# Optimization experiments

Hardware: AMD Instinct MI355X
Metric: run time of the kernel (lower is better)

## Reference

```python
import jax, jax.numpy as jnp
import numpy as np

A, N, D, H, ADIM = 8, 32768, 128, 4, 32  # agents, batch, hidden, heads, attend_dim


def setup_inputs() -> dict:
    key = jax.random.key(0)
    ks = jax.random.split(key, 7)
    querys = jax.random.normal(ks[0], (A, N, D), jnp.float32)
    keys = jax.random.normal(ks[1], (A, N, D), jnp.float32)
    values = jax.random.normal(ks[2], (A, N, D), jnp.float32)
    s = 1.0 / np.sqrt(D)
    Wk = jax.random.normal(ks[3], (H, ADIM, D), jnp.float32) * s   # key_extractors (no bias)
    Wsel = jax.random.normal(ks[4], (H, ADIM, D), jnp.float32) * s  # selector_extractors (no bias)
    Wv = jax.random.normal(ks[5], (H, ADIM, D), jnp.float32) * s   # value_extractors Linear
    bv = jax.random.normal(ks[6], (H, ADIM), jnp.float32) * s      # value_extractors bias
    return {"querys": querys, "keys": keys, "values": values,
            "Wk": Wk, "Wsel": Wsel, "Wv": Wv, "bv": bv}


def _offdiag_idx(a):
    # idx[i, j] enumerates the a-1 agents != i, in order (matches torch list comp j != a_i)
    j = jnp.arange(a - 1)[None, :]
    i = jnp.arange(a)[:, None]
    return jnp.where(j < i, j, j + 1)  # [A, A-1]


def reference(querys, keys, values, Wk, Wsel, Wv, bv):
    # per-head projections: [H, A, N, K]
    hk = jnp.einsum('and,hkd->hank', keys, Wk)
    hs = jnp.einsum('and,hkd->hank', querys, Wsel)
    hv = jax.nn.leaky_relu(jnp.einsum('and,hkd->hank', values, Wv) + bv[:, None, None, :],
                           negative_slope=0.01)
    # full logits over all key-agents j for each query-agent i: [H, A, N, A]
    logits_full = jnp.einsum('hink,hjnk->hinj', hs, hk)
    scale = 1.0 / jnp.sqrt(jnp.asarray(hk.shape[-1], hk.dtype))
    # self-exclusion: mask j == i so softmax over j equals softmax over the other agents
    self_mask = jnp.eye(A, dtype=bool)[None, :, None, :]
    probs_full = jax.nn.softmax(jnp.where(self_mask, -1e9, logits_full * scale), axis=-1)
    # attended values: [H, A, N, K] (diagonal prob is exactly 0 after masking? it is ~e^{-1e9} ~ 0)
    other = jnp.einsum('hinj,hjnk->hink', probs_full, hv)
    # gather the self-excluded logits/probs in the original (A-1)-length layout
    idx = _offdiag_idx(A)
    idx4 = jnp.broadcast_to(idx[None, :, None, :], logits_full.shape[:-1] + (A - 1,))
    logits_ex = jnp.take_along_axis(logits_full, idx4, axis=-1)  # [H, A, N, A-1]
    probs_ex = jnp.take_along_axis(probs_full, idx4, axis=-1)    # [H, A, N, A-1]
    # reorder to agent-major like the torch nested lists: [A, H, ...]
    return (jnp.swapaxes(other, 0, 1),
            jnp.swapaxes(logits_ex, 0, 1),
            jnp.swapaxes(probs_ex, 0, 1))
```

## Files before the change

kernel.cpp:

```cpp
#include <hip/hip_runtime.h>
#include <hip/hip_bf16.h>

typedef unsigned short u16;
typedef unsigned int u32;

#define AGT 8
#define NBATCH 32768
#define DDIM 128
#define HEADS 4
#define KDIM 32

typedef float f32x4 __attribute__((ext_vector_type(4)));
typedef __bf16 bf16x8 __attribute__((ext_vector_type(8)));
typedef short s16x8 __attribute__((ext_vector_type(8)));
typedef u32 u32x4 __attribute__((ext_vector_type(4)));

union FragU { s16x8 s; bf16x8 b; u32x4 u; };

__device__ __forceinline__ u16 f2bf(float f) {
  u32 u = __float_as_uint(f);
  u = (u + 0x7FFFu + ((u >> 16) & 1u)) >> 16;
  return (u16)u;
}

__global__ void prep_weights(const float* __restrict__ Wk,
                             const float* __restrict__ Ws,
                             const float* __restrict__ Wv,
                             u16* __restrict__ Wb) {
  int idx = blockIdx.x * 256 + threadIdx.x;
  if (idx >= 3 * 8 * 4 * 64 * 8) return;
  int b  = idx & 7;
  int l  = (idx >> 3) & 63;
  int kc = (idx >> 9) & 3;
  int t  = (idx >> 11) & 7;
  int pj = idx >> 14;
  int c = t * 16 + (l & 15);
  int h = c >> 5, kk = c & 31;
  int d = kc * 32 + ((b >> 2) << 4) + ((l >> 4) << 2) + (b & 3);
  const float* W = (pj == 0) ? Wk : ((pj == 1) ? Ws : Wv);
  Wb[idx] = f2bf(W[(h * KDIM + kk) * DDIM + d]);
}

__device__ __forceinline__ void issue8(const float* __restrict__ rowp, int lg,
                                       float4 r[8]) {
#pragma unroll
  for (int kc = 0; kc < 4; ++kc) {
    r[kc * 2]     = *(const float4*)(rowp + kc * 32 + lg * 4);
    r[kc * 2 + 1] = *(const float4*)(rowp + kc * 32 + lg * 4 + 16);
  }
}

__device__ __forceinline__ void cvt8(const float4 r[8], FragU f[4]) {
#pragma unroll
  for (int kc = 0; kc < 4; ++kc) {
    const float4 x0 = r[kc * 2];
    const float4 x1 = r[kc * 2 + 1];
    FragU t;
    t.b[0] = (__bf16)x0.x; t.b[1] = (__bf16)x0.y;
    t.b[2] = (__bf16)x0.z; t.b[3] = (__bf16)x0.w;
    t.b[4] = (__bf16)x1.x; t.b[5] = (__bf16)x1.y;
    t.b[6] = (__bf16)x1.z; t.b[7] = (__bf16)x1.w;
    f[kc] = t;
  }
}

__device__ __forceinline__ FragU pack2(const f32x4 lo, const f32x4 hi) {
  FragU t;
  t.b[0] = (__bf16)lo[0]; t.b[1] = (__bf16)lo[1];
  t.b[2] = (__bf16)lo[2]; t.b[3] = (__bf16)lo[3];
  t.b[4] = (__bf16)hi[0]; t.b[5] = (__bf16)hi[1];
  t.b[6] = (__bf16)hi[2]; t.b[7] = (__bf16)hi[3];
  return t;
}

template <int PJ>
__device__ __forceinline__ void projT2(const FragU fx0[4], const FragU fx1[4],
                                       const u16* __restrict__ Wb, int l,
                                       FragU o0[HEADS], FragU o1[HEADS]) {
  const f32x4 z = (f32x4)(0.0f);
#pragma unroll
  for (int g = 0; g < 2; ++g) {
    f32x4 a0[4], a1[4];
#pragma unroll
    for (int m4 = 0; m4 < 4; ++m4) {
      a0[m4] = z;
      a1[m4] = z;
      const int mt = g * 4 + m4;
#pragma unroll
      for (int kc = 0; kc < 4; ++kc) {
        FragU fb;
        fb.s = *(const s16x8*)(Wb + ((((PJ * 8 + mt) * 4 + kc) * 64 + l) << 3));
        a0[m4] = __builtin_amdgcn_mfma_f32_16x16x32_bf16(fb.b, fx0[kc].b,
                                                         a0[m4], 0, 0, 0);
        a1[m4] = __builtin_amdgcn_mfma_f32_16x16x32_bf16(fb.b, fx1[kc].b,
                                                         a1[m4], 0, 0, 0);
      }
    }
#pragma unroll
    for (int hh = 0; hh < 2; ++hh) {
      o0[g * 2 + hh] = pack2(a0[2 * hh], a0[2 * hh + 1]);
      o1[g * 2 + hh] = pack2(a1[2 * hh], a1[2 * hh + 1]);
    }
  }
}

__device__ __forceinline__ void projV2(const FragU fx0[4], const FragU fx1[4],
                                       const u16* __restrict__ Wb, int l,
                                       const float biasr[8],
                                       u32 hv0[8][2], u32 hv1[8][2]) {
  const f32x4 z = (f32x4)(0.0f);
#pragma unroll
  for (int ct = 0; ct < 8; ++ct) {
    f32x4 a0 = z, a1 = z;
#pragma unroll
    for (int kc = 0; kc < 4; ++kc) {
      FragU fb;
      fb.s = *(const s16x8*)(Wb + ((((16 + ct) * 4 + kc) * 64 + l) << 3));
      a0 = __builtin_amdgcn_mfma_f32_16x16x32_bf16(fx0[kc].b, fb.b, a0, 0, 0, 0);
      a1 = __builtin_amdgcn_mfma_f32_16x16x32_bf16(fx1[kc].b, fb.b, a1, 0, 0, 0);
    }
    const float bb = biasr[ct];
    {
      float x0 = a0[0] + bb, x1 = a0[1] + bb, x2 = a0[2] + bb, x3 = a0[3] + bb;
      x0 = (x0 > 0.f) ? x0 : 0.01f * x0;
      x1 = (x1 > 0.f) ? x1 : 0.01f * x1;
      x2 = (x2 > 0.f) ? x2 : 0.01f * x2;
      x3 = (x3 > 0.f) ? x3 : 0.01f * x3;
      FragU t;
      t.b[0] = (__bf16)x0; t.b[1] = (__bf16)x1;
      t.b[2] = (__bf16)x2; t.b[3] = (__bf16)x3;
      hv0[ct][0] = t.u[0];
      hv0[ct][1] = t.u[1];
    }
    {
      float x0 = a1[0] + bb, x1 = a1[1] + bb, x2 = a1[2] + bb, x3 = a1[3] + bb;
      x0 = (x0 > 0.f) ? x0 : 0.01f * x0;
      x1 = (x1 > 0.f) ? x1 : 0.01f * x1;
      x2 = (x2 > 0.f) ? x2 : 0.01f * x2;
      x3 = (x3 > 0.f) ? x3 : 0.01f * x3;
      FragU t;
      t.b[0] = (__bf16)x0; t.b[1] = (__bf16)x1;
      t.b[2] = (__bf16)x2; t.b[3] = (__bf16)x3;
      hv1[ct][0] = t.u[0];
      hv1[ct][1] = t.u[1];
    }
  }
}

__global__ __launch_bounds__(256, 3) void fused_attn(
    const float* __restrict__ qin, const float* __restrict__ kin,
    const float* __restrict__ vin, const u16* __restrict__ Wb,
    const float* __restrict__ bv,
    float* __restrict__ out0, float* __restrict__ out1,
    float* __restrict__ out2) {
  const int tid = threadIdx.x;
  const int l = tid & 63;
  const int w = tid >> 6;
  const int lr = l & 15;
  const int lg = l >> 4;
  const int nbase = (blockIdx.x * 4 + w) * 4;
  const int my_agent = lr >> 1;
  const int ipar = lr & 1;
  const size_t xoff0 =
      ((size_t)my_agent * NBATCH + (size_t)(nbase + ipar)) * DDIM;
  const size_t xoff1 = xoff0 + 2 * DDIM;

  float biasr[8];
#pragma unroll
  for (int ct = 0; ct < 8; ++ct) biasr[ct] = bv[ct * 16 + lr];

  const f32x4 zero4 = (f32x4)(0.0f);
  const float scale = 0.17677669529663687f;

  FragU hk[2][HEADS], hs[2][HEADS];
  u32 hv[2][8][2];

  {
    float4 rA[8], rB[8];
    issue8(kin + xoff0, lg, rA);
    issue8(kin + xoff1, lg, rB);
    FragU fx0[4], fx1[4];
    cvt8(rA, fx0);
    cvt8(rB, fx1);
    projT2<0>(fx0, fx1, Wb, l, hk[0], hk[1]);
  }
  {
    float4 rA[8], rB[8];
    issue8(qin + xoff0, lg, rA);
    issue8(qin + xoff1, lg, rB);
    FragU fx0[4], fx1[4];
    cvt8(rA, fx0);
    cvt8(rB, fx1);
    projT2<1>(fx0, fx1, Wb, l, hs[0], hs[1]);
  }
  {
    float4 rA[8], rB[8];
    issue8(vin + xoff0, lg, rA);
    issue8(vin + xoff1, lg, rB);
    FragU fx0[4], fx1[4];
    cvt8(rA, fx0);
    cvt8(rB, fx1);
    projV2(fx0, fx1, Wb, l, biasr, hv[0], hv[1]);
  }

  f32x4 S[2][HEADS];
#pragma unroll
  for (int t = 0; t < 2; ++t)
#pragma unroll
    for (int h = 0; h < HEADS; ++h)
      S[t][h] = __builtin_amdgcn_mfma_f32_16x16x32_bf16(hk[t][h].b, hs[t][h].b,
                                                        zero4, 0, 0, 0);

  const int a_i = my_agent;
#pragma unroll
  for (int t = 0; t < 2; ++t) {
    const int n_i = nbase + 2 * t + ipar;
#pragma unroll
    for (int h = 0; h < HEADS; ++h) {
      float sl[4];
#pragma unroll
      for (int rg = 0; rg < 4; ++rg) {
        const int jrow = 4 * lg + rg;
        const bool valid = ((rg & 1) == ipar) && (jrow != lr);
        sl[rg] = valid ? S[t][h][rg] * scale : -1e30f;
      }
      float mp = fmaxf(fmaxf(sl[0], sl[1]), fmaxf(sl[2], sl[3]));
      mp = fmaxf(mp, __shfl_xor(mp, 16));
      mp = fmaxf(mp, __shfl_xor(mp, 32));
      float e[4];
      float sp = 0.0f;
#pragma unroll
      for (int rg = 0; rg < 4; ++rg) {
        e[rg] = __expf(sl[rg] - mp);
        sp += e[rg];
      }
      sp += __shfl_xor(sp, 16);
      sp += __shfl_xor(sp, 32);
      const float inv = 1.0f / sp;
      float p[4];
#pragma unroll
      for (int rg = 0; rg < 4; ++rg) p[rg] = e[rg] * inv;

      const size_t ob7 =
          ((size_t)(a_i * HEADS + h) * NBATCH + (size_t)n_i) * 7;
#pragma unroll
      for (int rg = 0; rg < 4; ++rg) {
        const int jrow = 4 * lg + rg;
        if (((rg & 1) == ipar) && (jrow != lr)) {
          const int a_j = jrow >> 1;
          const int jj = a_j - ((a_j > a_i) ? 1 : 0);
          out1[ob7 + jj] = S[t][h][rg];
          out2[ob7 + jj] = p[rg];
        }
      }

      FragU P;
      P.b[0] = (__bf16)p[0]; P.b[1] = (__bf16)p[1];
      P.b[2] = (__bf16)p[2]; P.b[3] = (__bf16)p[3];
      P.u[2] = 0;
      P.u[3] = 0;
      FragU B0, B1;
      B0.u[0] = hv[t][2 * h][0];     B0.u[1] = hv[t][2 * h][1];
      B0.u[2] = 0;                   B0.u[3] = 0;
      B1.u[0] = hv[t][2 * h + 1][0]; B1.u[1] = hv[t][2 * h + 1][1];
      B1.u[2] = 0;                   B1.u[3] = 0;
      f32x4 O0 = __builtin_amdgcn_mfma_f32_16x16x32_bf16(P.b, B0.b, zero4,
                                                         0, 0, 0);
      f32x4 O1 = __builtin_amdgcn_mfma_f32_16x16x32_bf16(P.b, B1.b, zero4,
                                                         0, 0, 0);
#pragma unroll
      for (int rg = 0; rg < 4; ++rg) {
        const int irow = 4 * lg + rg;
        const int a_o = irow >> 1;
        const int n_o = nbase + 2 * t + (irow & 1);
        const size_t o0 =
            ((size_t)(a_o * HEADS + h) * NBATCH + (size_t)n_o) * KDIM;
        out0[o0 + lr] = O0[rg];
        out0[o0 + 16 + lr] = O1[rg];
      }
    }
  }
}

extern "C" void kernel_launch(void* const* d_in, const int* in_sizes, int n_in,
                              void* d_out, int out_size, void* d_ws,
                              size_t ws_size, hipStream_t stream) {
  const float* qin = (const float*)d_in[0];
  const float* kin = (const float*)d_in[1];
  const float* vin = (const float*)d_in[2];
  const float* Wk  = (const float*)d_in[3];
  const float* Ws  = (const float*)d_in[4];
  const float* Wv  = (const float*)d_in[5];
  const float* bvp = (const float*)d_in[6];

  float* out0 = (float*)d_out;
  float* out1 = out0 + (size_t)AGT * HEADS * NBATCH * KDIM;
  float* out2 = out1 + (size_t)AGT * HEADS * NBATCH * 7;

  u16* Wb = (u16*)d_ws;

  prep_weights<<<dim3(192), dim3(256), 0, stream>>>(Wk, Ws, Wv, Wb);
  fused_attn<<<dim3(2048), dim3(256), 0, stream>>>(
      qin, kin, vin, Wb, bvp, out0, out1, out2);
}
```

Before: 232.2 us.

## Split fused attention into projection and attention kernels via bf16 workspace

```diff
diff --git a/kernel.cpp b/kernel.cpp
--- a/kernel.cpp
+++ b/kernel.cpp
@@ -11,6 +11,7 @@
 #define KDIM 32
 
 typedef float f32x4 __attribute__((ext_vector_type(4)));
+typedef float f32x2 __attribute__((ext_vector_type(2)));
 typedef __bf16 bf16x8 __attribute__((ext_vector_type(8)));
 typedef short s16x8 __attribute__((ext_vector_type(8)));
 typedef u32 u32x4 __attribute__((ext_vector_type(4)));
@@ -21,6 +22,13 @@
   u32 u = __float_as_uint(f);
   u = (u + 0x7FFFu + ((u >> 16) & 1u)) >> 16;
   return (u16)u;
+}
+
+__device__ __forceinline__ f32x2 bfpair(u32 u) {
+  f32x2 r;
+  r.x = __uint_as_float(u << 16);
+  r.y = __uint_as_float(u & 0xFFFF0000u);
+  return r;
 }
 
 __global__ void prep_weights(const float* __restrict__ Wk,
@@ -64,6 +72,156 @@
   }
 }
 
+__global__ __launch_bounds__(256, 4) void proj_kernel(
+    const float* __restrict__ qin, const float* __restrict__ kin,
+    const float* __restrict__ vin, const u16* __restrict__ Wb,
+    const float* __restrict__ bv, u16* __restrict__ Y) {
+  const int tid = threadIdx.x;
+  const int l = tid & 63;
+  const int w = tid >> 6;
+  const int lr = l & 15;
+  const int lg = l >> 4;
+
+  const int gw = blockIdx.x * 4 + w;
+  const int pj = gw >> 13;
+  const int tile = gw & 8191;
+  const int r0 = tile * 32;
+  const int a = r0 >> 15;
+  const int n0 = r0 & (NBATCH - 1);
+
+  const float* X = (pj == 0) ? kin : ((pj == 1) ? qin : vin);
+  u16* Yp = Y + (size_t)pj * ((size_t)NBATCH * AGT * 128);
+
+  float4 rA[8], rB[8];
+  issue8(X + (size_t)(r0 + lr) * DDIM, lg, rA);
+  issue8(X + (size_t)(r0 + 16 + lr) * DDIM, lg, rB);
+  FragU fx0[4], fx1[4];
+  cvt8(rA, fx0);
+  cvt8(rB, fx1);
+
+  const f32x4 z = (f32x4)(0.0f);
+  const float bias = (pj == 2) ? bv[0 * 16 + lr] : 0.0f;
+
+#pragma unroll
+  for (int ct = 0; ct < 8; ++ct) {
+    f32x4 a0 = z, a1 = z;
+#pragma unroll
+    for (int kc = 0; kc < 4; ++kc) {
+      FragU fb;
+      fb.s = *(const s16x8*)(Wb + ((((pj * 8 + ct) * 4 + kc) * 64 + l) << 3));
+      a0 = __builtin_amdgcn_mfma_f32_16x16x32_bf16(fx0[kc].b, fb.b, a0, 0, 0, 0);
+      a1 = __builtin_amdgcn_mfma_f32_16x16x32_bf16(fx1[kc].b, fb.b, a1, 0, 0, 0);
+    }
+    const int c = ct * 16 + lr;
+    if (pj == 2) {
+      const float bb = bv[c];
+#pragma unroll
+      for (int rg = 0; rg < 4; ++rg) {
+        float v0 = a0[rg] + bb;
+        a0[rg] = (v0 > 0.f) ? v0 : 0.01f * v0;
+        float v1 = a1[rg] + bb;
+        a1[rg] = (v1 > 0.f) ? v1 : 0.01f * v1;
+      }
+    }
+#pragma unroll
+    for (int rg = 0; rg < 4; ++rg) {
+      const int row = 4 * lg + rg;
+      Yp[((size_t)(n0 + row) * 8 + a) * 128 + c] = f2bf(a0[rg]);
+      Yp[((size_t)(n0 + 16 + row) * 8 + a) * 128 + c] = f2bf(a1[rg]);
+    }
+  }
+  (void)bias;
+}
+
+__global__ __launch_bounds__(256, 4) void attn_kernel(
+    const u16* __restrict__ Y, float* __restrict__ out0,
+    float* __restrict__ out1, float* __restrict__ out2) {
+  const int tid = threadIdx.x;
+  const int i = tid & 7;
+  const int h = (tid >> 3) & 3;
+  const int n = blockIdx.x * 8 + (tid >> 5);
+
+  const size_t PST = (size_t)NBATCH * AGT * 128;
+  const u16* Yk = Y;
+  const u16* Ys = Y + PST;
+  const u16* Yv = Y + 2 * PST;
+  const int cb = h * 32;
+
+  f32x2 hs2[16];
+  {
+    const u16* p = Ys + ((size_t)n * 8 + i) * 128 + cb;
+#pragma unroll
+    for (int q = 0; q < 4; ++q) {
+      u32x4 ch = *(const u32x4*)(p + q * 8);
+#pragma unroll
+      for (int e = 0; e < 4; ++e) hs2[q * 4 + e] = bfpair(ch[e]);
+    }
+  }
+
+  float logits[8];
+#pragma unroll
+  for (int j = 0; j < 8; ++j) {
+    const u16* p = Yk + ((size_t)n * 8 + j) * 128 + cb;
+    f32x2 a2 = (f32x2)(0.0f);
+#pragma unroll
+    for (int q = 0; q < 4; ++q) {
+      u32x4 ch = *(const u32x4*)(p + q * 8);
+#pragma unroll
+      for (int e = 0; e < 4; ++e) a2 = bfpair(ch[e]) * hs2[q * 4 + e] + a2;
+    }
+    logits[j] = a2.x + a2.y;
+  }
+
+  const float scale = 0.17677669529663687f;
+  float sl[8];
+#pragma unroll
+  for (int j = 0; j < 8; ++j) sl[j] = (j == i) ? -1e30f : logits[j] * scale;
+  float m = sl[0];
+#pragma unroll
+  for (int j = 1; j < 8; ++j) m = fmaxf(m, sl[j]);
+  float p[8];
+  float s = 0.0f;
+#pragma unroll
+  for (int j = 0; j < 8; ++j) { p[j] = __expf(sl[j] - m); s += p[j]; }
+  const float inv = 1.0f / s;
+
+  const size_t ob = ((size_t)(i * HEADS + h) * NBATCH + (size_t)n);
+  const size_t ob7 = ob * 7;
+#pragma unroll
+  for (int j = 0; j < 8; ++j) {
+    if (j != i) {
+      const int jj = j - ((j > i) ? 1 : 0);
+      out1[ob7 + jj] = logits[j];
+      out2[ob7 + jj] = p[j] * inv;
+    }
+  }
+
+  f32x2 o2[16];
+#pragma unroll
+  for (int e = 0; e < 16; ++e) o2[e] = (f32x2)(0.0f);
+#pragma unroll
+  for (int j = 0; j < 8; ++j) {
+    const float pw = p[j] * inv;
+    const f32x2 pw2 = (f32x2)(pw);
+    const u16* vp = Yv + ((size_t)n * 8 + j) * 128 + cb;
+#pragma unroll
+    for (int q = 0; q < 4; ++q) {
+      u32x4 ch = *(const u32x4*)(vp + q * 8);
+#pragma unroll
+      for (int e = 0; e < 4; ++e)
+        o2[q * 4 + e] = bfpair(ch[e]) * pw2 + o2[q * 4 + e];
+    }
+  }
+
+  const size_t o0 = ob * 32;
+#pragma unroll
+  for (int g = 0; g < 8; ++g) {
+    float4 vv = make_float4(o2[g * 2].x, o2[g * 2].y,
+                            o2[g * 2 + 1].x, o2[g * 2 + 1].y);
+    *(float4*)(out0 + o0 + g * 4) = vv;
+  }
+}
+
 __device__ __forceinline__ FragU pack2(const f32x4 lo, const f32x4 hi) {
   FragU t;
   t.b[0] = (__bf16)lo[0]; t.b[1] = (__bf16)lo[1];
@@ -147,7 +305,7 @@
   }
 }
 
-__global__ __launch_bounds__(256, 3) void fused_attn(
+__global__ __launch_bounds__(256, 3) void fused_attn_fb(
     const float* __restrict__ qin, const float* __restrict__ kin,
     const float* __restrict__ vin, const u16* __restrict__ Wb,
     const float* __restrict__ bv,
@@ -298,8 +456,20 @@
   float* out2 = out1 + (size_t)AGT * HEADS * NBATCH * 7;
 
   u16* Wb = (u16*)d_ws;
+  const size_t WB_ELEMS = 49152;
+  const size_t Y_ELEMS = (size_t)3 * NBATCH * AGT * 128;
+  const size_t NEED = (WB_ELEMS + Y_ELEMS) * sizeof(u16);
 
   prep_weights<<<dim3(192), dim3(256), 0, stream>>>(Wk, Ws, Wv, Wb);
-  fused_attn<<<dim3(2048), dim3(256), 0, stream>>>(
-      qin, kin, vin, Wb, bvp, out0, out1, out2);
-}
+
+  if (ws_size >= NEED) {
+    u16* Y = Wb + WB_ELEMS;
+    proj_kernel<<<dim3(6144), dim3(256), 0, stream>>>(qin, kin, vin, Wb, bvp,
+                                                      Y);
+    attn_kernel<<<dim3(NBATCH / 8), dim3(256), 0, stream>>>(Y, out0, out1,
+                                                            out2);
+  } else {
+    fused_attn_fb<<<dim3(2048), dim3(256), 0, stream>>>(
+        qin, kin, vin, Wb, bvp, out0, out1, out2);
+  }
+}
```

Result: slower. 349.3 us (+50.4%).
